# Performance work log

Hardware: AMD Instinct MI355X
Metric: run time of the kernel (lower is better)

Reference implementation:

```python
import jax, jax.numpy as jnp
import numpy as np

D_MODEL = 1024
NHEAD = 16
D_K = D_MODEL // NHEAD
EPS_ATTN = 1e-6
EPS_LN = 1e-5


def _linear(k, fan_in, fan_out):
    k1, k2 = jax.random.split(k)
    bound = 1.0 / np.sqrt(fan_in)
    W = jax.random.uniform(k1, (fan_out, fan_in), jnp.float32, -bound, bound)
    b = jax.random.uniform(k2, (fan_out,), jnp.float32, -bound, bound)
    return W, b


def setup_inputs() -> dict:
    key = jax.random.key(0)
    ks = jax.random.split(key, 8)
    src = jax.random.normal(ks[0], (4096, 4, D_MODEL), jnp.float32)
    Wq, bq = _linear(ks[1], D_MODEL, D_MODEL)
    Wk, bk = _linear(ks[2], D_MODEL, D_MODEL)
    Wv, bv = _linear(ks[3], D_MODEL, D_MODEL)
    Wo, bo = _linear(ks[4], D_MODEL, D_MODEL)
    W1, b1 = _linear(ks[5], D_MODEL, 2 * D_MODEL)
    W2, b2 = _linear(ks[6], 2 * D_MODEL, D_MODEL)
    g1 = jnp.ones((D_MODEL,), jnp.float32)
    be1 = jnp.zeros((D_MODEL,), jnp.float32)
    g2 = jnp.ones((D_MODEL,), jnp.float32)
    be2 = jnp.zeros((D_MODEL,), jnp.float32)
    return {"src": src, "Wq": Wq, "bq": bq, "Wk": Wk, "bk": bk, "Wv": Wv, "bv": bv,
            "Wo": Wo, "bo": bo, "W1": W1, "b1": b1, "W2": W2, "b2": b2,
            "g1": g1, "be1": be1, "g2": g2, "be2": be2}


def _layernorm(x, g, b):
    mu = jnp.mean(x, axis=-1, keepdims=True)
    var = jnp.mean(jnp.square(x - mu), axis=-1, keepdims=True)
    return (x - mu) * jax.lax.rsqrt(var + EPS_LN) * g + b


def reference(src, Wq, bq, Wk, bk, Wv, bv, Wo, bo, W1, b1, W2, b2, g1, be1, g2, be2):
    S, B, D = src.shape
    Q = src @ Wq.T + bq  # [S,B,D]
    K = src @ Wk.T + bk
    V = src @ Wv.T + bv
    # split heads: [S,B,H,dk]
    Q = Q.reshape(S, B, NHEAD, D_K)
    K = K.reshape(S, B, NHEAD, D_K)
    V = V.reshape(S, B, NHEAD, D_K)
    phiQ = jax.nn.elu(Q) + 1.0
    phiK = jax.nn.elu(K) + 1.0
    # context per (batch, head): [B,H,dk,dk]
    context = jnp.einsum('sbhd,sbhe->bhde', phiK, V)
    out = jnp.einsum('sbhd,bhde->sbhe', phiQ, context)
    denom = jnp.einsum('sbhd,bhd->sbh', phiQ, phiK.sum(axis=0))
    out = out / (denom[..., None] + EPS_ATTN)
    attn = out.reshape(S, B, D)  # concat heads
    out = attn @ Wo.T + bo  # dropout = identity (eval)
    out = _layernorm(src + out, g1, be1)
    ffn = jax.nn.relu(out @ W1.T + b1) @ W2.T + b2
    out = _layernorm(out + ffn, g2, be2)
    return out
```

## Files before the change

kernel.cpp:

```cpp
#include <hip/hip_runtime.h>
#include <hip/hip_bf16.h>

typedef __hip_bfloat16 bf16;
typedef __attribute__((ext_vector_type(4))) float floatx4;
typedef __attribute__((ext_vector_type(8))) short shortx8;

#define MFMA16(a, b, c) __builtin_amdgcn_mfma_f32_16x16x32_bf16(a, b, c, 0, 0, 0)

__device__ __forceinline__ void gll16(const bf16* g, void* l) {
  __builtin_amdgcn_global_load_lds((const __attribute__((address_space(1))) unsigned int*)g,
                                   (__attribute__((address_space(3))) unsigned int*)l,
                                   16, 0, 0);
}

__device__ __forceinline__ shortx8 ds8(const char* p) {
  shortx8 r;
  unsigned a = (unsigned)(unsigned long long)(const __attribute__((address_space(3))) char*)p;
  asm volatile("ds_read_b128 %0, %1" : "=v"(r) : "v"(a));
  return r;
}

__device__ __forceinline__ float b2f(short s) {
  return __bfloat162float(__builtin_bit_cast(bf16, (unsigned short)s));
}
__device__ __forceinline__ short f2b(float f) {
  return __builtin_bit_cast(short, __float2bfloat16(f));
}

__global__ __launch_bounds__(256) void f2b_all(
    const float* __restrict__ src, const float* __restrict__ Wq,
    const float* __restrict__ Wk, const float* __restrict__ Wv,
    const float* __restrict__ Wo, const float* __restrict__ W1,
    const float* __restrict__ W2, bf16* __restrict__ src_bf,
    bf16* __restrict__ Wq_b, bf16* __restrict__ Wk_b, bf16* __restrict__ Wv_b,
    bf16* __restrict__ Wo_b, bf16* __restrict__ W1_b, bf16* __restrict__ W2_b) {
  const int blk = blockIdx.x;
  const float* in;
  bf16* out;
  int off;
  if (blk < 16384)      { in = src; out = src_bf; off = blk; }
  else if (blk < 17408) { in = Wq; out = Wq_b; off = blk - 16384; }
  else if (blk < 18432) { in = Wk; out = Wk_b; off = blk - 17408; }
  else if (blk < 19456) { in = Wv; out = Wv_b; off = blk - 18432; }
  else if (blk < 20480) { in = Wo; out = Wo_b; off = blk - 19456; }
  else if (blk < 22528) { in = W1; out = W1_b; off = blk - 20480; }
  else                  { in = W2; out = W2_b; off = blk - 22528; }
  const int i = (off * 256 + threadIdx.x) * 4;
  float4 v = *(const float4*)(in + i);
  ushort4 u;
  u.x = (unsigned short)f2b(v.x);
  u.y = (unsigned short)f2b(v.y);
  u.z = (unsigned short)f2b(v.z);
  u.w = (unsigned short)f2b(v.w);
  *(ushort4*)(out + i) = u;
}

template <int EPI>
__global__ __launch_bounds__(512, 2) void gemm256(
    const bf16* __restrict__ A, const bf16* __restrict__ Bw,
    const float* __restrict__ bias0, const float* __restrict__ bias1,
    const float* __restrict__ bias2, const float* __restrict__ resf,
    const bf16* __restrict__ resb, void* __restrict__ out0,
    void* __restrict__ out1, void* __restrict__ out2, const int M,
    const int K) {
  __shared__ __align__(16) char smem[131072];
  const int tid = threadIdx.x;
  const int lane = tid & 63, wave = tid >> 6;
  const int wm = wave & 1, wn = wave >> 1;
  const int bm = blockIdx.x, bn = blockIdx.y;
  const int NK = K >> 5;

  const int srow = tid >> 2;
  const int schunk = (tid & 3) ^ ((srow >> 1) & 3);
  const bf16* gA0 = A + (size_t)(bm * 256 + srow) * K + schunk * 8;
  const bf16* gA1 = gA0 + (size_t)128 * K;
  const bf16* gB0 = Bw + (size_t)(bn * 256 + srow) * K + schunk * 8;
  const bf16* gB1 = gB0 + (size_t)128 * K;
  const unsigned ldst = (unsigned)wave * 1024u;

  const int frow = lane & 15;
  const unsigned fch16 = (unsigned)(((lane >> 4) ^ ((frow >> 1) & 3))) << 4;
  const unsigned aoff0 = (unsigned)(wm * 8192 + frow * 64) + fch16;
  const unsigned boff0 = 65536u + (unsigned)(wn * 4096 + frow * 64) + fch16;

  floatx4 acc[8][4] = {};

#define STAGE_A(t)                                                       \
  {                                                                      \
    const int kk = (t) * 32;                                             \
    const unsigned bo = (unsigned)(((t) & 3) * 16384) + ldst;            \
    gll16(gA0 + kk, smem + bo);                                          \
    gll16(gA1 + kk, smem + bo + 8192);                                   \
  }
#define STAGE_B(t)                                                       \
  {                                                                      \
    const int kk = (t) * 32;                                             \
    const unsigned bo = 65536u + (unsigned)(((t) & 3) * 16384) + ldst;   \
    gll16(gB0 + kk, smem + bo);                                          \
    gll16(gB1 + kk, smem + bo + 8192);                                   \
  }

  STAGE_A(0); STAGE_B(0);
  STAGE_A(1); STAGE_B(1);
  STAGE_A(2); STAGE_B(2);
  asm volatile("s_waitcnt vmcnt(8)");
  __builtin_amdgcn_sched_barrier(0);
  __builtin_amdgcn_s_barrier();

  for (int kt = 0; kt < NK; ++kt) {
    const unsigned ab = aoff0 + (unsigned)((kt & 3) * 16384);
    const unsigned bb = boff0 + (unsigned)((kt & 3) * 16384);
    shortx8 bfr[4], af[4];
#pragma unroll
    for (int j = 0; j < 4; j++) bfr[j] = ds8(smem + bb + j * 1024);
#pragma unroll
    for (int i = 0; i < 4; i++) af[i] = ds8(smem + ab + i * 1024);
    if (kt + 3 < NK) STAGE_A(kt + 3);
    __builtin_amdgcn_s_barrier();
    asm volatile("s_waitcnt lgkmcnt(0)");
    __builtin_amdgcn_sched_barrier(0);
    __builtin_amdgcn_s_setprio(1);
#pragma unroll
    for (int i = 0; i < 4; i++)
#pragma unroll
      for (int j = 0; j < 4; j++) acc[i][j] = MFMA16(af[i], bfr[j], acc[i][j]);
    __builtin_amdgcn_s_setprio(0);
#pragma unroll
    for (int i = 0; i < 4; i++) af[i] = ds8(smem + ab + (4 + i) * 1024);
    if (kt + 3 < NK) STAGE_B(kt + 3);
    __builtin_amdgcn_s_barrier();
    asm volatile("s_waitcnt lgkmcnt(0)");
    __builtin_amdgcn_sched_barrier(0);
    __builtin_amdgcn_s_setprio(1);
#pragma unroll
    for (int i = 0; i < 4; i++)
#pragma unroll
      for (int j = 0; j < 4; j++)
        acc[4 + i][j] = MFMA16(af[i], bfr[j], acc[4 + i][j]);
    __builtin_amdgcn_s_setprio(0);
    if (kt < NK - 1) {
      if (kt < NK - 3) {
        asm volatile("s_waitcnt vmcnt(8)");
      } else if (kt == NK - 3) {
        asm volatile("s_waitcnt vmcnt(4)");
      } else {
        asm volatile("s_waitcnt vmcnt(0)");
      }
      __builtin_amdgcn_sched_barrier(0);
      __builtin_amdgcn_s_barrier();
    }
  }
#undef STAGE_A
#undef STAGE_B

  bf16* cep = (bf16*)smem;
  const float* bptr = bias0;
  bf16* ob = (bf16*)out0;
  int colbase = bn * 256;
  int phi = 0;
  if (EPI == 4) {
    const int sel = bn >> 2;
    bptr = (sel == 0) ? bias0 : (sel == 1) ? bias1 : bias2;
    ob = (bf16*)((sel == 0) ? out0 : (sel == 1) ? out1 : out2);
    colbase = (bn & 3) * 256;
    phi = (sel < 2);
  }
  const int e = lane & 15, q4 = (lane >> 4) << 2;
  float bj[4];
#pragma unroll
  for (int j = 0; j < 4; j++) bj[j] = bptr[colbase + wn * 64 + j * 16 + e];

  const int ridx = tid >> 4;
  const int cc = (tid & 15) * 8;
  const int grow_base = bm * 256 + (ridx >> 4) * 128 + (ridx & 15);

#pragma unroll
  for (int i = 0; i < 8; i++) {
    __syncthreads();
#pragma unroll
    for (int j = 0; j < 4; j++)
#pragma unroll
      for (int r = 0; r < 4; r++) {
        float v = acc[i][j][r] + bj[j];
        if (EPI == 4 && phi) v = v > 0.f ? v + 1.f : __expf(v);
        if (EPI == 2) v = fmaxf(v, 0.f);
        cep[(wm * 16 + q4 + r) * 264 + wn * 64 + j * 16 + e] =
            __builtin_bit_cast(bf16, f2b(v));
      }
    __syncthreads();
    const int grow = grow_base + i * 16;
#pragma unroll
    for (int h = 0; h < 2; h++) {
      const int col = cc + h * 128;
      shortx8 v = *(const shortx8*)&cep[ridx * 264 + col];
      if (EPI == 3) {
        const float* rp = resf + (size_t)grow * M + colbase + col;
        float4 r0 = *(const float4*)rp;
        float4 r1 = *(const float4*)(rp + 4);
        v[0] = f2b(b2f(v[0]) + r0.x); v[1] = f2b(b2f(v[1]) + r0.y);
        v[2] = f2b(b2f(v[2]) + r0.z); v[3] = f2b(b2f(v[3]) + r0.w);
        v[4] = f2b(b2f(v[4]) + r1.x); v[5] = f2b(b2f(v[5]) + r1.y);
        v[6] = f2b(b2f(v[6]) + r1.z); v[7] = f2b(b2f(v[7]) + r1.w);
      } else if (EPI == 5) {
        shortx8 rv = *(const shortx8*)(resb + (size_t)grow * M + colbase + col);
#pragma unroll
        for (int k = 0; k < 8; k++) v[k] = f2b(b2f(v[k]) + b2f(rv[k]));
      }
      *(shortx8*)(ob + (size_t)grow * M + colbase + col) = v;
    }
  }
}

__global__ __launch_bounds__(256) void ctx_mfma(const bf16* __restrict__ phiK,
                                                const bf16* __restrict__ V,
                                                float* __restrict__ ctx,
                                                float* __restrict__ ksum) {
  __shared__ __align__(16) short sKT[64][72];
  __shared__ __align__(16) short sVT[64][72];
  const int bh = blockIdx.x, b = bh >> 4, h = bh & 15;
  const int t = threadIdx.x, lane = t & 63, wave = t >> 6;
  const int s_l = t >> 2;
  const int c0 = (t & 3) << 4;
  const int frow = lane & 15, fk = (lane >> 4) << 3;
  const shortx8 ones = (shortx8)(short)0x3F80;
  floatx4 acc[4] = {};
  floatx4 accK = {};

  const int sbeg = blockIdx.y * 512;
  for (int sub = 0; sub < 8; sub++) {
    const size_t g = ((size_t)(sbeg + sub * 64 + s_l) * 4 + b) * 1024 + h * 64 + c0;
    shortx8 kv0 = *(const shortx8*)(phiK + g);
    shortx8 kv1 = *(const shortx8*)(phiK + g + 8);
    shortx8 vv0 = *(const shortx8*)(V + g);
    shortx8 vv1 = *(const shortx8*)(V + g + 8);
    __syncthreads();
#pragma unroll
    for (int j = 0; j < 8; j++) {
      sKT[c0 + j][s_l] = kv0[j];
      sKT[c0 + 8 + j][s_l] = kv1[j];
      sVT[c0 + j][s_l] = vv0[j];
      sVT[c0 + 8 + j][s_l] = vv1[j];
    }
    __syncthreads();
#pragma unroll
    for (int ks = 0; ks < 2; ks++) {
      shortx8 af = *(const shortx8*)&sKT[wave * 16 + frow][ks * 32 + fk];
      accK = MFMA16(af, ones, accK);
#pragma unroll
      for (int j = 0; j < 4; j++) {
        shortx8 bfr = *(const shortx8*)&sVT[j * 16 + frow][ks * 32 + fk];
        acc[j] = MFMA16(af, bfr, acc[j]);
      }
    }
  }

  float* cdst = ctx + (size_t)bh * 4096;
  const int dr0 = wave * 16 + ((lane >> 4) << 2);
  const int e = lane & 15;
#pragma unroll
  for (int j = 0; j < 4; j++)
#pragma unroll
    for (int r = 0; r < 4; r++)
      atomicAdd(cdst + (size_t)(dr0 + r) * 64 + j * 16 + e, acc[j][r]);
  if (e == 0) {
#pragma unroll
    for (int r = 0; r < 4; r++) atomicAdd(ksum + bh * 64 + dr0 + r, accK[r]);
  }
}

__global__ __launch_bounds__(256) void attn_mfma(const bf16* __restrict__ phiQ,
                                                 const float* __restrict__ ctx,
                                                 const float* __restrict__ ksum,
                                                 bf16* __restrict__ attn) {
  __shared__ __align__(16) bf16 sctxT[64][72];
  __shared__ __align__(16) bf16 sks[64];
  const int bh = blockIdx.x, b = bh >> 4, h = bh & 15;
  const int t = threadIdx.x, lane = t & 63, wave = t >> 6;
  const float* cbase = ctx + (size_t)bh * 4096;
  for (int idx = t; idx < 4096; idx += 256) {
    int d = idx >> 6, e = idx & 63;
    sctxT[e][d] = __float2bfloat16(cbase[idx]);
  }
  if (t < 64) sks[t] = __float2bfloat16(ksum[bh * 64 + t]);
  __syncthreads();

  const int s0 = blockIdx.y * 128 + wave * 32;
  const int frow = lane & 15, fk = (lane >> 4) << 3;
  shortx8 bfr[2][4], kfr[2];
#pragma unroll
  for (int ks = 0; ks < 2; ks++) {
#pragma unroll
    for (int j = 0; j < 4; j++) bfr[ks][j] = *(const shortx8*)&sctxT[j * 16 + frow][ks * 32 + fk];
    kfr[ks] = *(const shortx8*)&sks[ks * 32 + fk];
  }
  floatx4 acc[2][4] = {};
  floatx4 accd[2] = {};
#pragma unroll
  for (int i = 0; i < 2; i++) {
#pragma unroll
    for (int ks = 0; ks < 2; ks++) {
      const int srow = s0 + i * 16 + frow;
      const bf16* ap = phiQ + ((size_t)srow * 4 + b) * 1024 + h * 64 + ks * 32 + fk;
      shortx8 af = *(const shortx8*)ap;
#pragma unroll
      for (int j = 0; j < 4; j++) acc[i][j] = MFMA16(af, bfr[ks][j], acc[i][j]);
      accd[i] = MFMA16(af, kfr[ks], accd[i]);
    }
  }
#pragma unroll
  for (int i = 0; i < 2; i++) {
#pragma unroll
    for (int r = 0; r < 4; r++) {
      const int srow = s0 + i * 16 + ((lane >> 4) << 2) + r;
      const float den = accd[i][r] + 1e-6f;
#pragma unroll
      for (int j = 0; j < 4; j++) {
        const int e = j * 16 + (lane & 15);
        attn[((size_t)srow * 4 + b) * 1024 + h * 64 + e] = __float2bfloat16(acc[i][j][r] / den);
      }
    }
  }
}

__global__ __launch_bounds__(256) void ln_kernel(const bf16* __restrict__ x,
                                                 const float* __restrict__ g,
                                                 const float* __restrict__ be,
                                                 bf16* __restrict__ outb,
                                                 float* __restrict__ outf) {
  const int row = blockIdx.x, t = threadIdx.x;
  const ushort4 u = ((const ushort4*)(x + (size_t)row * 1024))[t];
  float v0 = b2f((short)u.x), v1 = b2f((short)u.y);
  float v2 = b2f((short)u.z), v3 = b2f((short)u.w);
  float s = v0 + v1 + v2 + v3;
  float q = v0 * v0 + v1 * v1 + v2 * v2 + v3 * v3;
#pragma unroll
  for (int off = 32; off; off >>= 1) {
    s += __shfl_xor(s, off);
    q += __shfl_xor(q, off);
  }
  __shared__ float ss[4], sq[4];
  const int wave = t >> 6;
  if ((t & 63) == 0) { ss[wave] = s; sq[wave] = q; }
  __syncthreads();
  s = ss[0] + ss[1] + ss[2] + ss[3];
  q = sq[0] + sq[1] + sq[2] + sq[3];
  const float mu = s * (1.f / 1024.f);
  const float var = q * (1.f / 1024.f) - mu * mu;
  const float rstd = rsqrtf(var + 1e-5f);
  const float4 gv = ((const float4*)g)[t];
  const float4 bv = ((const float4*)be)[t];
  float y0 = (v0 - mu) * rstd * gv.x + bv.x;
  float y1 = (v1 - mu) * rstd * gv.y + bv.y;
  float y2 = (v2 - mu) * rstd * gv.z + bv.z;
  float y3 = (v3 - mu) * rstd * gv.w + bv.w;
  if (outb != nullptr) {
    ushort4 o;
    o.x = (unsigned short)f2b(y0); o.y = (unsigned short)f2b(y1);
    o.z = (unsigned short)f2b(y2); o.w = (unsigned short)f2b(y3);
    ((ushort4*)(outb + (size_t)row * 1024))[t] = o;
  } else {
    float4 o = {y0, y1, y2, y3};
    ((float4*)(outf + (size_t)row * 1024))[t] = o;
  }
}

extern "C" void kernel_launch(void* const* d_in, const int* in_sizes, int n_in,
                              void* d_out, int out_size, void* d_ws, size_t ws_size,
                              hipStream_t stream) {
  const float* src = (const float*)d_in[0];
  const float* Wq = (const float*)d_in[1];
  const float* bq = (const float*)d_in[2];
  const float* Wk = (const float*)d_in[3];
  const float* bk = (const float*)d_in[4];
  const float* Wv = (const float*)d_in[5];
  const float* bv = (const float*)d_in[6];
  const float* Wo = (const float*)d_in[7];
  const float* bo = (const float*)d_in[8];
  const float* W1 = (const float*)d_in[9];
  const float* b1 = (const float*)d_in[10];
  const float* W2 = (const float*)d_in[11];
  const float* b2 = (const float*)d_in[12];
  const float* g1 = (const float*)d_in[13];
  const float* be1 = (const float*)d_in[14];
  const float* g2 = (const float*)d_in[15];
  const float* be2 = (const float*)d_in[16];

  const size_t MB = 1024 * 1024;
  char* w = (char*)d_ws;
  bf16* src_bf = (bf16*)(w + 0);
  bf16* x1b = (bf16*)(w + 0);
  bf16* phiQ = (bf16*)(w + 64 * MB);
  bf16* phiK = (bf16*)(w + 96 * MB);
  bf16* attn = (bf16*)(w + 96 * MB);
  bf16* Vb = (bf16*)(w + 128 * MB);
  bf16* out1b = (bf16*)(w + 128 * MB);
  bf16* x2b = (bf16*)(w + 160 * MB);
  bf16* Wq_b = (bf16*)(w + 224 * MB);
  bf16* Wk_b = (bf16*)(w + 226 * MB);
  bf16* Wv_b = (bf16*)(w + 228 * MB);
  bf16* Wo_b = (bf16*)(w + 230 * MB);
  bf16* W1_b = (bf16*)(w + 232 * MB);
  bf16* W2_b = (bf16*)(w + 236 * MB);
  float* ctx = (float*)(w + 240 * MB);
  float* ksum = (float*)(w + 241 * MB);
  bf16* H1 = (bf16*)d_out;
  float* outf = (float*)d_out;

  const dim3 blk(256), blk5(512);
  f2b_all<<<24576, blk, 0, stream>>>(src, Wq, Wk, Wv, Wo, W1, W2, src_bf, Wq_b,
                                     Wk_b, Wv_b, Wo_b, W1_b, W2_b);
  hipMemsetAsync(ctx, 0, (64 * 64 * 64 + 64 * 64) * sizeof(float), stream);

  gemm256<4><<<dim3(64, 12), blk5, 0, stream>>>(
      src_bf, Wq_b, bq, bk, bv, nullptr, nullptr, phiQ, phiK, Vb, 1024, 1024);
  ctx_mfma<<<dim3(64, 8), blk, 0, stream>>>(phiK, Vb, ctx, ksum);
  attn_mfma<<<dim3(64, 32), blk, 0, stream>>>(phiQ, ctx, ksum, attn);
  gemm256<3><<<dim3(64, 4), blk5, 0, stream>>>(
      attn, Wo_b, bo, nullptr, nullptr, src, nullptr, x1b, nullptr, nullptr, 1024, 1024);
  ln_kernel<<<16384, blk, 0, stream>>>(x1b, g1, be1, out1b, nullptr);
  gemm256<2><<<dim3(64, 8), blk5, 0, stream>>>(
      out1b, W1_b, b1, nullptr, nullptr, nullptr, nullptr, H1, nullptr, nullptr, 2048, 1024);
  gemm256<5><<<dim3(64, 4), blk5, 0, stream>>>(
      H1, W2_b, b2, nullptr, nullptr, nullptr, out1b, x2b, nullptr, nullptr, 1024, 2048);
  ln_kernel<<<16384, blk, 0, stream>>>(x2b, g2, be2, nullptr, outf);
}
```

Before: 532.8 us.

## Double-buffer GEMM register fragments with one barrier per k-tile

Restructures the GEMM main loop to use two sets of register fragments, unrolled by two k-tiles. The next tile's LDS fragment reads are issued while the current tile's MFMAs run, and the A and B global-to-LDS stages are merged so each k-tile needs one barrier instead of several. The goal is to hide LDS read latency and cut barrier stalls, at the cost of more vector registers and an assumption that the k-tile count is even. It also changes the epilogue staging row stride from 264 to 268 to reduce LDS bank conflicts, but this breaks 16-byte alignment of the vector reads.

```diff
diff --git a/kernel.cpp b/kernel.cpp
--- a/kernel.cpp
+++ b/kernel.cpp
@@ -84,6 +84,7 @@
   const unsigned boff0 = 65536u + (unsigned)(wn * 4096 + frow * 64) + fch16;
 
   floatx4 acc[8][4] = {};
+  shortx8 fa0[8], fa1[8], fb0[4], fb1[4];
 
 #define STAGE_A(t)                                                       \
   {                                                                      \
@@ -106,50 +107,58 @@
   asm volatile("s_waitcnt vmcnt(8)");
   __builtin_amdgcn_sched_barrier(0);
   __builtin_amdgcn_s_barrier();
-
-  for (int kt = 0; kt < NK; ++kt) {
-    const unsigned ab = aoff0 + (unsigned)((kt & 3) * 16384);
-    const unsigned bb = boff0 + (unsigned)((kt & 3) * 16384);
-    shortx8 bfr[4], af[4];
-#pragma unroll
-    for (int j = 0; j < 4; j++) bfr[j] = ds8(smem + bb + j * 1024);
-#pragma unroll
-    for (int i = 0; i < 4; i++) af[i] = ds8(smem + ab + i * 1024);
-    if (kt + 3 < NK) STAGE_A(kt + 3);
-    __builtin_amdgcn_s_barrier();
-    asm volatile("s_waitcnt lgkmcnt(0)");
-    __builtin_amdgcn_sched_barrier(0);
-    __builtin_amdgcn_s_setprio(1);
-#pragma unroll
-    for (int i = 0; i < 4; i++)
-#pragma unroll
-      for (int j = 0; j < 4; j++) acc[i][j] = MFMA16(af[i], bfr[j], acc[i][j]);
-    __builtin_amdgcn_s_setprio(0);
-#pragma unroll
-    for (int i = 0; i < 4; i++) af[i] = ds8(smem + ab + (4 + i) * 1024);
-    if (kt + 3 < NK) STAGE_B(kt + 3);
-    __builtin_amdgcn_s_barrier();
-    asm volatile("s_waitcnt lgkmcnt(0)");
-    __builtin_amdgcn_sched_barrier(0);
-    __builtin_amdgcn_s_setprio(1);
-#pragma unroll
-    for (int i = 0; i < 4; i++)
-#pragma unroll
-      for (int j = 0; j < 4; j++)
-        acc[4 + i][j] = MFMA16(af[i], bfr[j], acc[4 + i][j]);
-    __builtin_amdgcn_s_setprio(0);
-    if (kt < NK - 1) {
-      if (kt < NK - 3) {
-        asm volatile("s_waitcnt vmcnt(8)");
-      } else if (kt == NK - 3) {
-        asm volatile("s_waitcnt vmcnt(4)");
-      } else {
-        asm volatile("s_waitcnt vmcnt(0)");
-      }
-      __builtin_amdgcn_sched_barrier(0);
-      __builtin_amdgcn_s_barrier();
-    }
-  }
+  {
+#pragma unroll
+    for (int j = 0; j < 4; j++) fb0[j] = ds8(smem + boff0 + j * 1024);
+#pragma unroll
+    for (int i = 0; i < 4; i++) fa0[i] = ds8(smem + aoff0 + i * 1024);
+#pragma unroll
+    for (int i = 0; i < 4; i++) fa0[4 + i] = ds8(smem + aoff0 + (4 + i) * 1024);
+  }
+
+#define TILE_BODY(t, FAC, FBC, FAN, FBN)                                     \
+  {                                                                          \
+    asm volatile("s_waitcnt lgkmcnt(4)");                                    \
+    __builtin_amdgcn_sched_barrier(0);                                       \
+    __builtin_amdgcn_s_setprio(1);                                           \
+    _Pragma("unroll") for (int i = 0; i < 4; i++)                            \
+      _Pragma("unroll") for (int j = 0; j < 4; j++)                          \
+        acc[i][j] = MFMA16(FAC[i], FBC[j], acc[i][j]);                       \
+    __builtin_amdgcn_s_setprio(0);                                           \
+    if ((t) <= NK - 3) asm volatile("s_waitcnt vmcnt(4)");                   \
+    else               asm volatile("s_waitcnt vmcnt(0)");                   \
+    __builtin_amdgcn_sched_barrier(0);                                       \
+    __builtin_amdgcn_s_barrier();                                            \
+    if ((t) + 3 < NK) { STAGE_A((t) + 3); STAGE_B((t) + 3); }                \
+    if ((t) + 1 < NK) {                                                      \
+      const unsigned ab = aoff0 + (unsigned)(((((t) + 1)) & 3) * 16384);     \
+      const unsigned bb = boff0 + (unsigned)(((((t) + 1)) & 3) * 16384);     \
+      _Pragma("unroll") for (int j = 0; j < 4; j++)                          \
+        FBN[j] = ds8(smem + bb + j * 1024);                                  \
+      _Pragma("unroll") for (int i = 0; i < 4; i++)                          \
+        FAN[i] = ds8(smem + ab + i * 1024);                                  \
+      asm volatile("s_waitcnt lgkmcnt(8)");                                  \
+    } else {                                                                 \
+      asm volatile("s_waitcnt lgkmcnt(0)");                                  \
+    }                                                                        \
+    __builtin_amdgcn_sched_barrier(0);                                       \
+    __builtin_amdgcn_s_setprio(1);                                           \
+    _Pragma("unroll") for (int i = 0; i < 4; i++)                            \
+      _Pragma("unroll") for (int j = 0; j < 4; j++)                          \
+        acc[4 + i][j] = MFMA16(FAC[4 + i], FBC[j], acc[4 + i][j]);           \
+    __builtin_amdgcn_s_setprio(0);                                           \
+    if ((t) + 1 < NK) {                                                      \
+      const unsigned ab = aoff0 + (unsigned)(((((t) + 1)) & 3) * 16384);     \
+      _Pragma("unroll") for (int i = 0; i < 4; i++)                          \
+        FAN[4 + i] = ds8(smem + ab + (4 + i) * 1024);                        \
+    }                                                                        \
+  }
+
+  for (int kt = 0; kt < NK; kt += 2) {
+    TILE_BODY(kt, fa0, fb0, fa1, fb1);
+    TILE_BODY(kt + 1, fa1, fb1, fa0, fb0);
+  }
+#undef TILE_BODY
 #undef STAGE_A
 #undef STAGE_B
 
@@ -184,7 +193,7 @@
         float v = acc[i][j][r] + bj[j];
         if (EPI == 4 && phi) v = v > 0.f ? v + 1.f : __expf(v);
         if (EPI == 2) v = fmaxf(v, 0.f);
-        cep[(wm * 16 + q4 + r) * 264 + wn * 64 + j * 16 + e] =
+        cep[(wm * 16 + q4 + r) * 268 + wn * 64 + j * 16 + e] =
             __builtin_bit_cast(bf16, f2b(v));
       }
     __syncthreads();
@@ -192,7 +201,7 @@
 #pragma unroll
     for (int h = 0; h < 2; h++) {
       const int col = cc + h * 128;
-      shortx8 v = *(const shortx8*)&cep[ridx * 264 + col];
+      shortx8 v = *(const shortx8*)&cep[ridx * 268 + col];
       if (EPI == 3) {
         const float* rp = resf + (size_t)grow * M + colbase + col;
         float4 r0 = *(const float4*)rp;
```

After: 539.8 us. No clear change (+1.3%).

## Restructure GEMM main loop into double-buffered 64-wide K tiles

Applied to the files above, without the earlier changes.

Replaces the 4-slot ring of 32-wide K tiles with two 64 KB buffers, each holding a 64-wide K tile split into two halves. Each iteration runs four MFMA sub-phases, with global-to-LDS loads for the next tiles interleaved between them. The aim is to halve the per-K-step waitcnt and barrier overhead and keep loads overlapped with MFMA work, at the cost of extra s_barriers per sub-phase. Separately, the epilogue LDS row stride changes from 264 to 268 to alter bank mapping. That makes 16-byte row reads start on 8-byte boundaries for odd rows, so alignment is a risk.

```diff
diff --git a/kernel.cpp b/kernel.cpp
--- a/kernel.cpp
+++ b/kernel.cpp
@@ -68,7 +68,7 @@
   const int lane = tid & 63, wave = tid >> 6;
   const int wm = wave & 1, wn = wave >> 1;
   const int bm = blockIdx.x, bn = blockIdx.y;
-  const int NK = K >> 5;
+  const int NT = K >> 6;
 
   const int srow = tid >> 2;
   const int schunk = (tid & 3) ^ ((srow >> 1) & 3);
@@ -80,42 +80,57 @@
 
   const int frow = lane & 15;
   const unsigned fch16 = (unsigned)(((lane >> 4) ^ ((frow >> 1) & 3))) << 4;
-  const unsigned aoff0 = (unsigned)(wm * 8192 + frow * 64) + fch16;
-  const unsigned boff0 = 65536u + (unsigned)(wn * 4096 + frow * 64) + fch16;
+  const unsigned aoff = (unsigned)(wm * 8192 + frow * 64) + fch16;
+  const unsigned boff = (unsigned)(wn * 4096 + frow * 64) + fch16;
 
   floatx4 acc[8][4] = {};
-
-#define STAGE_A(t)                                                       \
-  {                                                                      \
-    const int kk = (t) * 32;                                             \
-    const unsigned bo = (unsigned)(((t) & 3) * 16384) + ldst;            \
-    gll16(gA0 + kk, smem + bo);                                          \
-    gll16(gA1 + kk, smem + bo + 8192);                                   \
-  }
-#define STAGE_B(t)                                                       \
-  {                                                                      \
-    const int kk = (t) * 32;                                             \
-    const unsigned bo = 65536u + (unsigned)(((t) & 3) * 16384) + ldst;   \
-    gll16(gB0 + kk, smem + bo);                                          \
-    gll16(gB1 + kk, smem + bo + 8192);                                   \
-  }
-
-  STAGE_A(0); STAGE_B(0);
-  STAGE_A(1); STAGE_B(1);
-  STAGE_A(2); STAGE_B(2);
-  asm volatile("s_waitcnt vmcnt(8)");
+  shortx8 af[8], fb[4];
+
+#define ST_A0(tt)                                                            \
+  {                                                                          \
+    const unsigned bd = (unsigned)(((tt) & 1) * 65536);                      \
+    const int kk = (tt) * 64;                                                \
+    gll16(gA0 + kk, smem + bd + ldst);                                       \
+    gll16(gA1 + kk, smem + bd + 8192 + ldst);                                \
+  }
+#define ST_B0(tt)                                                            \
+  {                                                                          \
+    const unsigned bd = (unsigned)(((tt) & 1) * 65536);                      \
+    const int kk = (tt) * 64;                                                \
+    gll16(gB0 + kk, smem + bd + 16384 + ldst);                               \
+    gll16(gB1 + kk, smem + bd + 24576 + ldst);                               \
+  }
+#define ST_A1(tt)                                                            \
+  {                                                                          \
+    const unsigned bd = (unsigned)(((tt) & 1) * 65536);                      \
+    const int kk = (tt) * 64 + 32;                                           \
+    gll16(gA0 + kk, smem + bd + 32768 + ldst);                               \
+    gll16(gA1 + kk, smem + bd + 40960 + ldst);                               \
+  }
+#define ST_B1(tt)                                                            \
+  {                                                                          \
+    const unsigned bd = (unsigned)(((tt) & 1) * 65536);                      \
+    const int kk = (tt) * 64 + 32;                                           \
+    gll16(gB0 + kk, smem + bd + 49152 + ldst);                               \
+    gll16(gB1 + kk, smem + bd + 57344 + ldst);                               \
+  }
+
+  ST_A0(0); ST_B0(0); ST_A1(0); ST_B1(0); ST_A0(1); ST_B0(1);
+  asm volatile("s_waitcnt vmcnt(4)");
   __builtin_amdgcn_sched_barrier(0);
   __builtin_amdgcn_s_barrier();
 
-  for (int kt = 0; kt < NK; ++kt) {
-    const unsigned ab = aoff0 + (unsigned)((kt & 3) * 16384);
-    const unsigned bb = boff0 + (unsigned)((kt & 3) * 16384);
-    shortx8 bfr[4], af[4];
-#pragma unroll
-    for (int j = 0; j < 4; j++) bfr[j] = ds8(smem + bb + j * 1024);
-#pragma unroll
-    for (int i = 0; i < 4; i++) af[i] = ds8(smem + ab + i * 1024);
-    if (kt + 3 < NK) STAGE_A(kt + 3);
+  for (int t = 0; t < NT; ++t) {
+    const unsigned base = (unsigned)((t & 1) * 65536);
+    const unsigned ab0 = base + aoff;
+    const unsigned bb0 = base + 16384 + boff;
+    const unsigned ab1 = base + 32768 + aoff;
+    const unsigned bb1 = base + 49152 + boff;
+#pragma unroll
+    for (int j = 0; j < 4; j++) fb[j] = ds8(smem + bb0 + j * 1024);
+#pragma unroll
+    for (int i = 0; i < 4; i++) af[i] = ds8(smem + ab0 + i * 1024);
+    if (t + 1 < NT) ST_A1(t + 1);
     __builtin_amdgcn_s_barrier();
     asm volatile("s_waitcnt lgkmcnt(0)");
     __builtin_amdgcn_sched_barrier(0);
@@ -123,11 +138,12 @@
 #pragma unroll
     for (int i = 0; i < 4; i++)
 #pragma unroll
-      for (int j = 0; j < 4; j++) acc[i][j] = MFMA16(af[i], bfr[j], acc[i][j]);
+      for (int j = 0; j < 4; j++) acc[i][j] = MFMA16(af[i], fb[j], acc[i][j]);
     __builtin_amdgcn_s_setprio(0);
-#pragma unroll
-    for (int i = 0; i < 4; i++) af[i] = ds8(smem + ab + (4 + i) * 1024);
-    if (kt + 3 < NK) STAGE_B(kt + 3);
+    __builtin_amdgcn_s_barrier();
+#pragma unroll
+    for (int i = 0; i < 4; i++) af[4 + i] = ds8(smem + ab0 + (4 + i) * 1024);
+    if (t + 1 < NT) ST_B1(t + 1);
     __builtin_amdgcn_s_barrier();
     asm volatile("s_waitcnt lgkmcnt(0)");
     __builtin_amdgcn_sched_barrier(0);
@@ -136,22 +152,46 @@
     for (int i = 0; i < 4; i++)
 #pragma unroll
       for (int j = 0; j < 4; j++)
-        acc[4 + i][j] = MFMA16(af[i], bfr[j], acc[4 + i][j]);
+        acc[4 + i][j] = MFMA16(af[4 + i], fb[j], acc[4 + i][j]);
     __builtin_amdgcn_s_setprio(0);
-    if (kt < NK - 1) {
-      if (kt < NK - 3) {
-        asm volatile("s_waitcnt vmcnt(8)");
-      } else if (kt == NK - 3) {
-        asm volatile("s_waitcnt vmcnt(4)");
-      } else {
-        asm volatile("s_waitcnt vmcnt(0)");
-      }
-      __builtin_amdgcn_sched_barrier(0);
-      __builtin_amdgcn_s_barrier();
-    }
-  }
-#undef STAGE_A
-#undef STAGE_B
+    __builtin_amdgcn_s_barrier();
+#pragma unroll
+    for (int j = 0; j < 4; j++) fb[j] = ds8(smem + bb1 + j * 1024);
+#pragma unroll
+    for (int i = 0; i < 4; i++) af[i] = ds8(smem + ab1 + i * 1024);
+    if (t + 2 < NT) ST_A0(t + 2);
+    __builtin_amdgcn_s_barrier();
+    asm volatile("s_waitcnt lgkmcnt(0)");
+    __builtin_amdgcn_sched_barrier(0);
+    __builtin_amdgcn_s_setprio(1);
+#pragma unroll
+    for (int i = 0; i < 4; i++)
+#pragma unroll
+      for (int j = 0; j < 4; j++) acc[i][j] = MFMA16(af[i], fb[j], acc[i][j]);
+    __builtin_amdgcn_s_setprio(0);
+    __builtin_amdgcn_s_barrier();
+#pragma unroll
+    for (int i = 0; i < 4; i++) af[4 + i] = ds8(smem + ab1 + (4 + i) * 1024);
+    if (t + 2 < NT) ST_B0(t + 2);
+    __builtin_amdgcn_s_barrier();
+    asm volatile("s_waitcnt lgkmcnt(0)");
+    __builtin_amdgcn_sched_barrier(0);
+    __builtin_amdgcn_s_setprio(1);
+#pragma unroll
+    for (int i = 0; i < 4; i++)
+#pragma unroll
+      for (int j = 0; j < 4; j++)
+        acc[4 + i][j] = MFMA16(af[4 + i], fb[j], acc[4 + i][j]);
+    __builtin_amdgcn_s_setprio(0);
+    if (t < NT - 2)      asm volatile("s_waitcnt vmcnt(4)");
+    else                 asm volatile("s_waitcnt vmcnt(0)");
+    __builtin_amdgcn_sched_barrier(0);
+    __builtin_amdgcn_s_barrier();
+  }
+#undef ST_A0
+#undef ST_B0
+#undef ST_A1
+#undef ST_B1
 
   bf16* cep = (bf16*)smem;
   const float* bptr = bias0;
@@ -184,7 +224,7 @@
         float v = acc[i][j][r] + bj[j];
         if (EPI == 4 && phi) v = v > 0.f ? v + 1.f : __expf(v);
         if (EPI == 2) v = fmaxf(v, 0.f);
-        cep[(wm * 16 + q4 + r) * 264 + wn * 64 + j * 16 + e] =
+        cep[(wm * 16 + q4 + r) * 268 + wn * 64 + j * 16 + e] =
             __builtin_bit_cast(bf16, f2b(v));
       }
     __syncthreads();
@@ -192,7 +232,7 @@
 #pragma unroll
     for (int h = 0; h < 2; h++) {
       const int col = cc + h * 128;
-      shortx8 v = *(const shortx8*)&cep[ridx * 264 + col];
+      shortx8 v = *(const shortx8*)&cep[ridx * 268 + col];
       if (EPI == 3) {
         const float* rp = resf + (size_t)grow * M + colbase + col;
         float4 r0 = *(const float4*)rp;
```

After: 528.0 us. No clear change (-0.9%).
